# Performance work log

Hardware: AMD Instinct MI355X
Metric: run time of the kernel (lower is better)

## Reference

```python
import jax, jax.numpy as jnp
import numpy as np

N_NODES = 200000
IN_FEAT = 500
EMB = 128
HID = 64
N_CLASSES = 7


def setup_inputs() -> dict:
    key = jax.random.key(0)
    ks = jax.random.split(key, 7)
    scale = 0.05
    return {
        "adj": jnp.zeros((N_NODES,), dtype=jnp.float32),  # unused in pretrain path
        "features": jax.random.normal(ks[0], (N_NODES, IN_FEAT), dtype=jnp.float32),
        "W_emb": jax.random.normal(ks[1], (IN_FEAT, EMB), dtype=jnp.float32) * scale,
        "b_emb": jax.random.normal(ks[2], (EMB,), dtype=jnp.float32) * scale,
        "W_rt1": jax.random.normal(ks[3], (EMB, HID), dtype=jnp.float32) * scale,
        "b_rt1": jax.random.normal(ks[4], (HID,), dtype=jnp.float32) * scale,
        "W_rt2": jax.random.normal(ks[5], (HID, N_CLASSES), dtype=jnp.float32) * scale,
        "b_rt2": jax.random.normal(ks[6], (N_CLASSES,), dtype=jnp.float32) * scale,
    }


def reference(adj, features, W_emb, b_emb, W_rt1, b_rt1, W_rt2, b_rt2):
    # Policy.forward with pretrain=True:
    #   feature = ReLU(features @ W_emb + b_emb)        (get_embedding)
    #   res = (ReLU(feature @ W_rt1 + b_rt1)) @ W_rt2 + b_rt2   (get_rt, act='relu')
    emb = jax.nn.relu(features @ W_emb + b_emb)      # [N, EMB]
    h = jax.nn.relu(emb @ W_rt1 + b_rt1)             # [N, HID]
    return h @ W_rt2 + b_rt2                         # [N, N_CLASSES]
```

## Files before the change

kernel.cpp:

```cpp
#include <hip/hip_runtime.h>
#include <hip/hip_bf16.h>

typedef unsigned short u16;
typedef __bf16 bf16x8 __attribute__((ext_vector_type(8)));
typedef float f32x4 __attribute__((ext_vector_type(4)));

#define N_NODES 200000
#define IN_FEAT 500
#define EMB 128
#define HID 64
#define NC 7
#define BM 64
#define KPAD 512

#define FS 40
#define WS 40
#define W1S 136
#define ES 136
#define HS 72
#define W2S 72

#define WS_WT1_OFF (128*512)
#define WS_WT2_OFF (128*512 + 64*128)
#define WS_TOTAL   (128*512 + 64*128 + 16*64)

__device__ __forceinline__ u16 cvt_bf16(float v) {
    __hip_bfloat16 h = __float2bfloat16(v);
    return *(u16*)&h;
}

__global__ __launch_bounds__(256) void prep_weights(
    const float* __restrict__ W_emb, const float* __restrict__ W_rt1,
    const float* __restrict__ W_rt2, u16* __restrict__ ws)
{
    int idx = blockIdx.x * 256 + threadIdx.x;
    float v;
    bool ok = true;
    if (idx < 128*512) {
        int n = idx >> 9, k = idx & 511;
        v = (k < IN_FEAT) ? W_emb[k*EMB + n] : 0.f;
    } else if (idx < WS_WT2_OFF) {
        int j = idx - WS_WT1_OFF;
        int n = j >> 7, k = j & 127;
        v = W_rt1[k*HID + n];
    } else if (idx < WS_TOTAL) {
        int j = idx - WS_WT2_OFF;
        int n = j >> 6, k = j & 63;
        v = (n < NC) ? W_rt2[k*NC + n] : 0.f;
    } else {
        ok = false;
        v = 0.f;
    }
    if (ok) ws[idx] = cvt_bf16(v);
}

__global__ __launch_bounds__(256) void mlp_fused(
    const float* __restrict__ F, const u16* __restrict__ Wt_emb,
    const u16* __restrict__ Wt1g, const u16* __restrict__ Wt2g,
    const float* __restrict__ b_emb, const float* __restrict__ b1,
    const float* __restrict__ b2, float* __restrict__ out)
{
    __shared__ u16 Fch[BM * FS];
    __shared__ u16 Wch[EMB * WS];
    __shared__ u16 W1l[HID * W1S];
    __shared__ u16 W2l[16 * W2S];
    __shared__ u16 Et[BM * ES];
    __shared__ u16 Ht[BM * HS];

    const int tid  = threadIdx.x;
    const int wave = tid >> 6;
    const int lane = tid & 63;
    const int l15  = lane & 15;
    const int q    = lane >> 4;
    const int row0 = blockIdx.x * BM;

    #pragma unroll
    for (int i = 0; i < 4; ++i) {
        int g = tid * 4 + i;
        int r = g >> 4, cc = (g & 15) * 8;
        *(uint4*)&W1l[r*W1S + cc] = *(const uint4*)&Wt1g[r*128 + cc];
    }
    if (tid < 128) {
        int r = tid >> 3, cc = (tid & 7) * 8;
        *(uint4*)&W2l[r*W2S + cc] = *(const uint4*)&Wt2g[r*64 + cc];
    }

    f32x4 acc[8];
    #pragma unroll
    for (int t = 0; t < 8; ++t) acc[t] = (f32x4){0.f,0.f,0.f,0.f};

    for (int c = 0; c < 16; ++c) {
        const int k0 = c * 32;
        {
            int r = tid >> 2, g = tid & 3;
            const float* src = F + (size_t)(row0 + r) * IN_FEAT + k0 + g * 8;
            union { u16 u[8]; uint4 v4; } pk;
            if (c < 15 || g < 2) {
                float4 f0 = *(const float4*)(src);
                float4 f1 = *(const float4*)(src + 4);
                pk.u[0] = cvt_bf16(f0.x); pk.u[1] = cvt_bf16(f0.y);
                pk.u[2] = cvt_bf16(f0.z); pk.u[3] = cvt_bf16(f0.w);
                pk.u[4] = cvt_bf16(f1.x); pk.u[5] = cvt_bf16(f1.y);
                pk.u[6] = cvt_bf16(f1.z); pk.u[7] = cvt_bf16(f1.w);
            } else {
                #pragma unroll
                for (int j = 0; j < 8; ++j) {
                    int k = k0 + g * 8 + j;
                    pk.u[j] = (k < IN_FEAT) ? cvt_bf16(src[j]) : (u16)0;
                }
            }
            *(uint4*)&Fch[r*FS + g*8] = pk.v4;
        }
        {
            int n = tid >> 1, h = (tid & 1) * 16;
            *(uint4*)&Wch[n*WS + h]     = *(const uint4*)&Wt_emb[n*KPAD + k0 + h];
            *(uint4*)&Wch[n*WS + h + 8] = *(const uint4*)&Wt_emb[n*KPAD + k0 + h + 8];
        }
        __syncthreads();

        bf16x8 a = *(const bf16x8*)&Fch[(wave*16 + l15)*FS + q*8];
        #pragma unroll
        for (int t = 0; t < 8; ++t) {
            bf16x8 b = *(const bf16x8*)&Wch[(t*16 + l15)*WS + q*8];
            acc[t] = __builtin_amdgcn_mfma_f32_16x16x32_bf16(a, b, acc[t], 0, 0, 0);
        }
        __syncthreads();
    }

    #pragma unroll
    for (int t = 0; t < 8; ++t) {
        float bias = b_emb[t*16 + l15];
        #pragma unroll
        for (int r = 0; r < 4; ++r) {
            float v = acc[t][r] + bias;
            v = v > 0.f ? v : 0.f;
            Et[(wave*16 + q*4 + r)*ES + t*16 + l15] = cvt_bf16(v);
        }
    }
    __syncthreads();

    f32x4 acc2[4];
    #pragma unroll
    for (int t = 0; t < 4; ++t) acc2[t] = (f32x4){0.f,0.f,0.f,0.f};
    #pragma unroll
    for (int kc = 0; kc < 4; ++kc) {
        bf16x8 a = *(const bf16x8*)&Et[(wave*16 + l15)*ES + kc*32 + q*8];
        #pragma unroll
        for (int t = 0; t < 4; ++t) {
            bf16x8 b = *(const bf16x8*)&W1l[(t*16 + l15)*W1S + kc*32 + q*8];
            acc2[t] = __builtin_amdgcn_mfma_f32_16x16x32_bf16(a, b, acc2[t], 0, 0, 0);
        }
    }
    #pragma unroll
    for (int t = 0; t < 4; ++t) {
        float bias = b1[t*16 + l15];
        #pragma unroll
        for (int r = 0; r < 4; ++r) {
            float v = acc2[t][r] + bias;
            v = v > 0.f ? v : 0.f;
            Ht[(wave*16 + q*4 + r)*HS + t*16 + l15] = cvt_bf16(v);
        }
    }
    __syncthreads();

    f32x4 acc3 = (f32x4){0.f,0.f,0.f,0.f};
    #pragma unroll
    for (int kc = 0; kc < 2; ++kc) {
        bf16x8 a = *(const bf16x8*)&Ht[(wave*16 + l15)*HS + kc*32 + q*8];
        bf16x8 b = *(const bf16x8*)&W2l[l15*W2S + kc*32 + q*8];
        acc3 = __builtin_amdgcn_mfma_f32_16x16x32_bf16(a, b, acc3, 0, 0, 0);
    }
    if (l15 < NC) {
        float bias = b2[l15];
        #pragma unroll
        for (int r = 0; r < 4; ++r) {
            float v = acc3[r] + bias;
            out[(size_t)(row0 + wave*16 + q*4 + r) * NC + l15] = v;
        }
    }
}

extern "C" void kernel_launch(void* const* d_in, const int* in_sizes, int n_in,
                              void* d_out, int out_size, void* d_ws, size_t ws_size,
                              hipStream_t stream) {
    const float* F     = (const float*)d_in[1];
    const float* W_emb = (const float*)d_in[2];
    const float* b_emb = (const float*)d_in[3];
    const float* W_rt1 = (const float*)d_in[4];
    const float* b_rt1 = (const float*)d_in[5];
    const float* W_rt2 = (const float*)d_in[6];
    const float* b_rt2 = (const float*)d_in[7];
    u16* ws    = (u16*)d_ws;
    float* out = (float*)d_out;

    int prep_blocks = (WS_TOTAL + 255) / 256;
    prep_weights<<<prep_blocks, 256, 0, stream>>>(W_emb, W_rt1, W_rt2, ws);

    mlp_fused<<<N_NODES / BM, 256, 0, stream>>>(
        F, ws, ws + WS_WT1_OFF, ws + WS_WT2_OFF,
        b_emb, b_rt1, b_rt2, out);
}
```

Before: 594.5 us.

## Load features directly into registers, pre-swizzle W_emb, double rows per block

Removes the LDS staging and per-chunk __syncthreads of the first GEMM. Each lane now loads its own feature fragment straight from global memory with a one-step register prefetch. W_emb is pre-permuted into MFMA fragment order so each lane reads its B operand with one contiguous vector load, which should hit in cache. Block rows double to 128, each wave handling two 16-row tiles so every B fragment feeds two MFMAs. The costs are higher register pressure, fewer blocks, and per-lane feature loads that are less coalesced (rows strided by 2000 bytes).

```diff
diff --git a/kernel.cpp b/kernel.cpp
--- a/kernel.cpp
+++ b/kernel.cpp
@@ -10,11 +10,9 @@
 #define EMB 128
 #define HID 64
 #define NC 7
-#define BM 64
+#define BM 128
 #define KPAD 512
 
-#define FS 40
-#define WS 40
 #define W1S 136
 #define ES 136
 #define HS 72
@@ -27,6 +25,15 @@
 __device__ __forceinline__ u16 cvt_bf16(float v) {
     __hip_bfloat16 h = __float2bfloat16(v);
     return *(u16*)&h;
+}
+
+__device__ __forceinline__ bf16x8 cvt8(float4 a, float4 b) {
+    union { u16 u[8]; bf16x8 v; } pk;
+    pk.u[0] = cvt_bf16(a.x); pk.u[1] = cvt_bf16(a.y);
+    pk.u[2] = cvt_bf16(a.z); pk.u[3] = cvt_bf16(a.w);
+    pk.u[4] = cvt_bf16(b.x); pk.u[5] = cvt_bf16(b.y);
+    pk.u[6] = cvt_bf16(b.z); pk.u[7] = cvt_bf16(b.w);
+    return pk.v;
 }
 
 __global__ __launch_bounds__(256) void prep_weights(
@@ -35,9 +42,13 @@
 {
     int idx = blockIdx.x * 256 + threadIdx.x;
     float v;
-    bool ok = true;
     if (idx < 128*512) {
-        int n = idx >> 9, k = idx & 511;
+        int j    = idx & 7;
+        int lane = (idx >> 3) & 63;
+        int t    = (idx >> 9) & 7;
+        int c    = idx >> 12;
+        int n = t*16 + (lane & 15);
+        int k = c*32 + (lane >> 4)*8 + j;
         v = (k < IN_FEAT) ? W_emb[k*EMB + n] : 0.f;
     } else if (idx < WS_WT2_OFF) {
         int j = idx - WS_WT1_OFF;
@@ -48,20 +59,17 @@
         int n = j >> 6, k = j & 63;
         v = (n < NC) ? W_rt2[k*NC + n] : 0.f;
     } else {
-        ok = false;
-        v = 0.f;
-    }
-    if (ok) ws[idx] = cvt_bf16(v);
+        return;
+    }
+    ws[idx] = cvt_bf16(v);
 }
 
 __global__ __launch_bounds__(256) void mlp_fused(
-    const float* __restrict__ F, const u16* __restrict__ Wt_emb,
+    const float* __restrict__ F, const u16* __restrict__ Wf,
     const u16* __restrict__ Wt1g, const u16* __restrict__ Wt2g,
     const float* __restrict__ b_emb, const float* __restrict__ b1,
     const float* __restrict__ b2, float* __restrict__ out)
 {
-    __shared__ u16 Fch[BM * FS];
-    __shared__ u16 Wch[EMB * WS];
     __shared__ u16 W1l[HID * W1S];
     __shared__ u16 W2l[16 * W2S];
     __shared__ u16 Et[BM * ES];
@@ -85,97 +93,121 @@
         *(uint4*)&W2l[r*W2S + cc] = *(const uint4*)&Wt2g[r*64 + cc];
     }
 
-    f32x4 acc[8];
-    #pragma unroll
-    for (int t = 0; t < 8; ++t) acc[t] = (f32x4){0.f,0.f,0.f,0.f};
+    int ra = row0 + wave*32 + l15;
+    int rb = ra + 16;
+    if (ra >= N_NODES) ra = N_NODES - 1;
+    if (rb >= N_NODES) rb = N_NODES - 1;
+    const float* p0 = F + (size_t)ra * IN_FEAT + q*8;
+    const float* p1 = F + (size_t)rb * IN_FEAT + q*8;
+    const u16*   wl = Wf + lane*8;
+
+    f32x4 acc[2][8];
+    #pragma unroll
+    for (int m = 0; m < 2; ++m)
+        #pragma unroll
+        for (int t = 0; t < 8; ++t) acc[m][t] = (f32x4){0.f,0.f,0.f,0.f};
+
+    float4 a0l = *(const float4*)(p0);
+    float4 a0h = *(const float4*)(p0 + 4);
+    float4 a1l = *(const float4*)(p1);
+    float4 a1h = *(const float4*)(p1 + 4);
 
     for (int c = 0; c < 16; ++c) {
-        const int k0 = c * 32;
-        {
-            int r = tid >> 2, g = tid & 3;
-            const float* src = F + (size_t)(row0 + r) * IN_FEAT + k0 + g * 8;
-            union { u16 u[8]; uint4 v4; } pk;
-            if (c < 15 || g < 2) {
-                float4 f0 = *(const float4*)(src);
-                float4 f1 = *(const float4*)(src + 4);
-                pk.u[0] = cvt_bf16(f0.x); pk.u[1] = cvt_bf16(f0.y);
-                pk.u[2] = cvt_bf16(f0.z); pk.u[3] = cvt_bf16(f0.w);
-                pk.u[4] = cvt_bf16(f1.x); pk.u[5] = cvt_bf16(f1.y);
-                pk.u[6] = cvt_bf16(f1.z); pk.u[7] = cvt_bf16(f1.w);
+        bf16x8 fa0 = cvt8(a0l, a0h);
+        bf16x8 fa1 = cvt8(a1l, a1h);
+
+        if (c < 15) {
+            const float* s0 = p0 + (c + 1) * 32;
+            const float* s1 = p1 + (c + 1) * 32;
+            if (c == 14) {
+                float4 z = make_float4(0.f, 0.f, 0.f, 0.f);
+                a0l = z; a0h = z; a1l = z; a1h = z;
+                if (q < 3) { a0l = *(const float4*)s0; a1l = *(const float4*)s1; }
+                if (q < 2) { a0h = *(const float4*)(s0 + 4);
+                             a1h = *(const float4*)(s1 + 4); }
             } else {
-                #pragma unroll
-                for (int j = 0; j < 8; ++j) {
-                    int k = k0 + g * 8 + j;
-                    pk.u[j] = (k < IN_FEAT) ? cvt_bf16(src[j]) : (u16)0;
-                }
-            }
-            *(uint4*)&Fch[r*FS + g*8] = pk.v4;
-        }
-        {
-            int n = tid >> 1, h = (tid & 1) * 16;
-            *(uint4*)&Wch[n*WS + h]     = *(const uint4*)&Wt_emb[n*KPAD + k0 + h];
-            *(uint4*)&Wch[n*WS + h + 8] = *(const uint4*)&Wt_emb[n*KPAD + k0 + h + 8];
-        }
-        __syncthreads();
-
-        bf16x8 a = *(const bf16x8*)&Fch[(wave*16 + l15)*FS + q*8];
+                a0l = *(const float4*)s0; a0h = *(const float4*)(s0 + 4);
+                a1l = *(const float4*)s1; a1h = *(const float4*)(s1 + 4);
+            }
+        }
+
+        const u16* wc = wl + c * 4096;
         #pragma unroll
         for (int t = 0; t < 8; ++t) {
-            bf16x8 b = *(const bf16x8*)&Wch[(t*16 + l15)*WS + q*8];
-            acc[t] = __builtin_amdgcn_mfma_f32_16x16x32_bf16(a, b, acc[t], 0, 0, 0);
-        }
-        __syncthreads();
+            bf16x8 b = *(const bf16x8*)(wc + t * 512);
+            acc[0][t] = __builtin_amdgcn_mfma_f32_16x16x32_bf16(fa0, b, acc[0][t], 0, 0, 0);
+            acc[1][t] = __builtin_amdgcn_mfma_f32_16x16x32_bf16(fa1, b, acc[1][t], 0, 0, 0);
+        }
     }
 
     #pragma unroll
     for (int t = 0; t < 8; ++t) {
         float bias = b_emb[t*16 + l15];
         #pragma unroll
-        for (int r = 0; r < 4; ++r) {
-            float v = acc[t][r] + bias;
-            v = v > 0.f ? v : 0.f;
-            Et[(wave*16 + q*4 + r)*ES + t*16 + l15] = cvt_bf16(v);
+        for (int m = 0; m < 2; ++m) {
+            #pragma unroll
+            for (int r = 0; r < 4; ++r) {
+                float v = acc[m][t][r] + bias;
+                v = v > 0.f ? v : 0.f;
+                Et[(wave*32 + m*16 + q*4 + r)*ES + t*16 + l15] = cvt_bf16(v);
+            }
         }
     }
     __syncthreads();
 
-    f32x4 acc2[4];
-    #pragma unroll
-    for (int t = 0; t < 4; ++t) acc2[t] = (f32x4){0.f,0.f,0.f,0.f};
+    f32x4 acc2[2][4];
+    #pragma unroll
+    for (int m = 0; m < 2; ++m)
+        #pragma unroll
+        for (int t = 0; t < 4; ++t) acc2[m][t] = (f32x4){0.f,0.f,0.f,0.f};
+
     #pragma unroll
     for (int kc = 0; kc < 4; ++kc) {
-        bf16x8 a = *(const bf16x8*)&Et[(wave*16 + l15)*ES + kc*32 + q*8];
+        bf16x8 a0 = *(const bf16x8*)&Et[(wave*32 +      l15)*ES + kc*32 + q*8];
+        bf16x8 a1 = *(const bf16x8*)&Et[(wave*32 + 16 + l15)*ES + kc*32 + q*8];
         #pragma unroll
         for (int t = 0; t < 4; ++t) {
             bf16x8 b = *(const bf16x8*)&W1l[(t*16 + l15)*W1S + kc*32 + q*8];
-            acc2[t] = __builtin_amdgcn_mfma_f32_16x16x32_bf16(a, b, acc2[t], 0, 0, 0);
+            acc2[0][t] = __builtin_amdgcn_mfma_f32_16x16x32_bf16(a0, b, acc2[0][t], 0, 0, 0);
+            acc2[1][t] = __builtin_amdgcn_mfma_f32_16x16x32_bf16(a1, b, acc2[1][t], 0, 0, 0);
         }
     }
     #pragma unroll
     for (int t = 0; t < 4; ++t) {
         float bias = b1[t*16 + l15];
         #pragma unroll
-        for (int r = 0; r < 4; ++r) {
-            float v = acc2[t][r] + bias;
-            v = v > 0.f ? v : 0.f;
-            Ht[(wave*16 + q*4 + r)*HS + t*16 + l15] = cvt_bf16(v);
+        for (int m = 0; m < 2; ++m) {
+            #pragma unroll
+            for (int r = 0; r < 4; ++r) {
+                float v = acc2[m][t][r] + bias;
+                v = v > 0.f ? v : 0.f;
+                Ht[(wave*32 + m*16 + q*4 + r)*HS + t*16 + l15] = cvt_bf16(v);
+            }
         }
     }
     __syncthreads();
 
-    f32x4 acc3 = (f32x4){0.f,0.f,0.f,0.f};
+    f32x4 acc3[2];
+    acc3[0] = (f32x4){0.f,0.f,0.f,0.f};
+    acc3[1] = (f32x4){0.f,0.f,0.f,0.f};
     #pragma unroll
     for (int kc = 0; kc < 2; ++kc) {
-        bf16x8 a = *(const bf16x8*)&Ht[(wave*16 + l15)*HS + kc*32 + q*8];
-        bf16x8 b = *(const bf16x8*)&W2l[l15*W2S + kc*32 + q*8];
-        acc3 = __builtin_amdgcn_mfma_f32_16x16x32_bf16(a, b, acc3, 0, 0, 0);
+        bf16x8 b  = *(const bf16x8*)&W2l[l15*W2S + kc*32 + q*8];
+        bf16x8 a0 = *(const bf16x8*)&Ht[(wave*32 +      l15)*HS + kc*32 + q*8];
+        bf16x8 a1 = *(const bf16x8*)&Ht[(wave*32 + 16 + l15)*HS + kc*32 + q*8];
+        acc3[0] = __builtin_amdgcn_mfma_f32_16x16x32_bf16(a0, b, acc3[0], 0, 0, 0);
+        acc3[1] = __builtin_amdgcn_mfma_f32_16x16x32_bf16(a1, b, acc3[1], 0, 0, 0);
     }
     if (l15 < NC) {
         float bias = b2[l15];
         #pragma unroll
-        for (int r = 0; r < 4; ++r) {
-            float v = acc3[r] + bias;
-            out[(size_t)(row0 + wave*16 + q*4 + r) * NC + l15] = v;
+        for (int m = 0; m < 2; ++m) {
+            #pragma unroll
+            for (int r = 0; r < 4; ++r) {
+                int row = row0 + wave*32 + m*16 + q*4 + r;
+                if (row < N_NODES)
+                    out[(size_t)row * NC + l15] = acc3[m][r] + bias;
+            }
         }
     }
 }
@@ -196,7 +228,8 @@
     int prep_blocks = (WS_TOTAL + 255) / 256;
     prep_weights<<<prep_blocks, 256, 0, stream>>>(W_emb, W_rt1, W_rt2, ws);
 
-    mlp_fused<<<N_NODES / BM, 256, 0, stream>>>(
+    int grid = (N_NODES + BM - 1) / BM;
+    mlp_fused<<<grid, 256, 0, stream>>>(
         F, ws, ws + WS_WT1_OFF, ws + WS_WT2_OFF,
         b_emb, b_rt1, b_rt2, out);
 }
```

Result: faster. 576.0 us (-3.1%).
